# Kernel optimization log

Hardware: AMD Instinct MI355X
Metric: run time of the kernel (lower is better)

## Reference

```python
import jax, jax.numpy as jnp
import numpy as np

B, T, EMB, H1, H2, NL, LMAX, VOCAB = 32, 20, 32, 64, 128, 4, 1024, 85
EPS = 1e-5

def _lengths():
    # ragged per-structure atom counts, max = 1024 (fixes pad length), sum = 24832
    return 1024 - np.arange(B) * 16

def _lstm(x, Wih0, Whh0, b0, WihS, WhhS, bS):
    """NL-layer batch-first LSTM, torch gate order (i,f,g,o), initial h/c = ones
    (matching the torch code's ones init states). Returns stacked final
    (h, c) per layer, each (NL, batch, hidden)."""
    n = x.shape[0]
    hidden = Whh0.shape[1]
    h_fin, c_fin = [], []
    inp = x
    for l in range(NL):
        Wih = Wih0 if l == 0 else WihS[l - 1]
        Whh = Whh0 if l == 0 else WhhS[l - 1]
        bb = b0 if l == 0 else bS[l - 1]
        xg = jnp.einsum('bti,gi->btg', inp, Wih) + bb  # (n, t, 4*hidden)
        init = (jnp.ones((n, hidden), x.dtype), jnp.ones((n, hidden), x.dtype))
        def step(carry, xt, Whh=Whh):
            h, c = carry
            g = xt + h @ Whh.T
            i, f, gg, o = jnp.split(g, 4, axis=-1)
            c = jax.nn.sigmoid(f) * c + jax.nn.sigmoid(i) * jnp.tanh(gg)
            h = jax.nn.sigmoid(o) * jnp.tanh(c)
            return (h, c), h
        (hT, cT), hs = jax.lax.scan(step, init, jnp.swapaxes(xg, 0, 1))
        inp = jnp.swapaxes(hs, 0, 1)
        h_fin.append(hT)
        c_fin.append(cT)
    return jnp.stack(h_fin), jnp.stack(c_fin)

def _bn_rows(x, g, b):
    # BatchNorm1d(batch_size) applied to x.T in torch: per-row (per-structure)
    # normalization over the feature axis, training-mode (biased var).
    m = x.mean(1, keepdims=True)
    v = x.var(1, keepdims=True)
    return (x - m) * jax.lax.rsqrt(v + EPS) * g[:, None] + b[:, None]

def setup_inputs():
    lengths = _lengths()
    N = int(lengths.sum())
    ks = jax.random.split(jax.random.key(0), 32)
    ki = iter(range(32))
    def nrm(shape, s):
        return s * jax.random.normal(ks[next(ki)], shape, jnp.float32)
    return {
        'neighbor_atom_batch': jax.random.randint(ks[next(ki)], (N * T,), 0, VOCAB, dtype=jnp.int32),
        'neighbors_distan_batch': jax.random.normal(ks[next(ki)], (N * T,), jnp.float32),
        'structure_num_bacth': jnp.asarray(lengths, jnp.int32),
        'batch_idx': jnp.asarray(np.repeat(np.arange(B), lengths), jnp.int32),
        'pos_idx': jnp.asarray(np.concatenate([np.arange(l) for l in lengths]), jnp.int32),
        'embed_w': nrm((VOCAB, EMB), 0.02),
        'l1_Wih0': nrm((4 * H1, EMB), 0.05), 'l1_Whh0': nrm((4 * H1, H1), 0.05), 'l1_b0': nrm((4 * H1,), 0.02),
        'l1_Wih': nrm((NL - 1, 4 * H1, H1), 0.05), 'l1_Whh': nrm((NL - 1, 4 * H1, H1), 0.05), 'l1_b': nrm((NL - 1, 4 * H1), 0.02),
        'l2_Wih0': nrm((4 * H2, H1), 0.05), 'l2_Whh0': nrm((4 * H2, H2), 0.05), 'l2_b0': nrm((4 * H2,), 0.02),
        'l2_Wih': nrm((NL - 1, 4 * H2, H2), 0.05), 'l2_Whh': nrm((NL - 1, 4 * H2, H2), 0.05), 'l2_b': nrm((NL - 1, 4 * H2), 0.02),
        'bn2_g': jnp.ones((B,), jnp.float32), 'bn2_b': jnp.zeros((B,), jnp.float32),
        'bn3_g': jnp.ones((B,), jnp.float32), 'bn3_b': jnp.zeros((B,), jnp.float32),
        'w1': nrm((128, 128), 0.1), 'b1': 0.1 * jnp.ones((128,), jnp.float32),
        'w2': nrm((64, 128), 0.1), 'b2': 0.1 * jnp.ones((64,), jnp.float32),
        'w22': nrm((64, 64), 0.1), 'b22': 0.1 * jnp.ones((64,), jnp.float32),
        'w3': nrm((32, 64), 0.1), 'b3': 0.1 * jnp.ones((32,), jnp.float32),
        'w4': nrm((32, 32), 0.1), 'b4': 0.1 * jnp.ones((32,), jnp.float32),
        'w5': nrm((16, 32), 0.1), 'b5': 0.1 * jnp.ones((16,), jnp.float32),
    }

def reference(neighbor_atom_batch, neighbors_distan_batch, structure_num_bacth,
              batch_idx, pos_idx, embed_w,
              l1_Wih0, l1_Whh0, l1_b0, l1_Wih, l1_Whh, l1_b,
              l2_Wih0, l2_Whh0, l2_b0, l2_Wih, l2_Whh, l2_b,
              bn2_g, bn2_b, bn3_g, bn3_b,
              w1, b1, w2, b2, w22, b22, w3, b3, w4, b4, w5, b5):
    # NOTE: neighbors_distan_batch is an argument of the torch forward but is
    # never used by its body; we keep it for signature fidelity.
    # embed, then scale each embedding row by its own integer atom id (as torch does)
    x = embed_w[neighbor_atom_batch] * neighbor_atom_batch.astype(jnp.float32)[:, None]
    x = x.reshape(-1, T, EMB)                       # (N, 20, 32)
    hT, cT = _lstm(x, l1_Wih0, l1_Whh0, l1_b0, l1_Wih, l1_Whh, l1_b)
    d = hT.mean(0) + cT.mean(0)                     # (N, 64)
    # ragged split by structure_num_bacth + pad_sequence -> (B, LMAX, 64), zero padded
    padded = jnp.zeros((B, LMAX, H1), d.dtype).at[batch_idx, pos_idx].set(d)
    # BatchNorm1d(batch_size): channel dim is the structure index -> stats over (len, feat)
    m = padded.mean((1, 2), keepdims=True)
    v = padded.var((1, 2), keepdims=True)
    padded = (padded - m) * jax.lax.rsqrt(v + EPS) * bn2_g[:, None, None] + bn2_b[:, None, None]
    _, cT2 = _lstm(padded, l2_Wih0, l2_Whh0, l2_b0, l2_Wih, l2_Whh, l2_b)
    d = cT2.mean(0)                                 # (B, 128) mean of final cell states
    d = _bn_rows(d, bn3_g, bn3_b)
    d = jax.nn.relu(d @ w1.T + b1)
    d = jax.nn.relu(d @ w2.T + b2)
    d = _bn_rows(d, bn3_g, bn3_b)                   # same BN layer reused, as in torch
    d = jax.nn.relu(d @ w22.T + b22)
    d = jax.nn.relu(d @ w3.T + b3)
    d = jax.nn.relu(d @ w4.T + b4)
    d = d @ w5.T + b5                               # (B, 16)
    return jax.nn.relu(d.sum(1))                    # (B,)
```

## Files before the change

### kernel.cpp

```cpp
#include <hip/hip_runtime.h>


typedef _Float16 f16x8  __attribute__((ext_vector_type(8)));
typedef float    f32x4  __attribute__((ext_vector_type(4)));

#define DEVI static __device__ __forceinline__

constexpr int   T1c   = 20;
constexpr int   EMBc  = 32;
constexpr int   H1c   = 64;
constexpr int   LMAXc = 1024;
constexpr int   VOCABc= 85;
constexpr int   Ntot  = 24832;
constexpr int   NTc   = Ntot * T1c;
constexpr int   R2c   = 32 * LMAXc;
constexpr float EPSc  = 1e-5f;

DEVI float sigm(float x)   { return 1.f / (1.f + __expf(-x)); }
DEVI float tanhf_(float x) { return 1.f - 2.f / (1.f + __expf(2.f * x)); }

DEVI void barrier_lds() {
    asm volatile("s_waitcnt lgkmcnt(0)\n\ts_barrier" ::: "memory");
}
DEVI void drain_vmem() {
    asm volatile("s_waitcnt vmcnt(0)" ::: "memory");
}

__global__ void __launch_bounds__(256)
k_prepw1(const float* __restrict__ Wih0, const float* __restrict__ Whh0,
         const float* __restrict__ WihS, const float* __restrict__ WhhS,
         _Float16* __restrict__ out)
{
    int i = blockIdx.x * 256 + threadIdx.x;
    if (i >= 4 * 256 * 128) return;
    int l = i >> 15, rem = i & 32767, r = rem >> 7, k = rem & 127;
    float v;
    if (l == 0) {
        if (k < 32)      v = Wih0[r * 32 + k];
        else if (k < 64) v = 0.f;
        else             v = Whh0[r * 64 + (k - 64)];
    } else {
        if (k < 64)      v = WihS[((l - 1) * 256 + r) * 64 + k];
        else             v = WhhS[((l - 1) * 256 + r) * 64 + (k - 64)];
    }
    out[i] = (_Float16)v;
}

__global__ void __launch_bounds__(256)
k_prepw2(const float* __restrict__ Wih0, const float* __restrict__ WihS,
         const float* __restrict__ Whh0, const float* __restrict__ WhhS,
         _Float16* __restrict__ wih, _Float16* __restrict__ whh,
         int* __restrict__ flags)
{
    int i = blockIdx.x * 256 + threadIdx.x;
    if (i < 512) flags[i] = (i < 256) ? 0 : 0x7fffffff;
    if (i >= 2 * 4 * 512 * 128) return;
    int half = i >> 18, rem = i & 262143;
    int l = rem >> 16, r = (rem >> 7) & 511, k = rem & 127;
    if (half == 0) {
        float v = (l == 0) ? ((k < 64) ? Wih0[r * 64 + k] : 0.f)
                           : WihS[((l - 1) * 512 + r) * 128 + k];
        wih[rem] = (_Float16)v;
    } else {
        float v = (l == 0) ? Whh0[r * 128 + k]
                           : WhhS[((l - 1) * 512 + r) * 128 + k];
        whh[rem] = (_Float16)v;
    }
}

__global__ void __launch_bounds__(256)
k_scan1all(const int* __restrict__ atoms, const float* __restrict__ ew,
           const _Float16* __restrict__ W16all,
           const float* __restrict__ b0, const float* __restrict__ bS,
           _Float16* __restrict__ seq, float* __restrict__ dacc)
{
    constexpr int SX = 136;
    __shared__ alignas(16) _Float16 xh[32 * SX];
    __shared__ float ewl[VOCABc * EMBc];
    __shared__ int   aidl[32 * T1c];

    const int tid  = threadIdx.x;
    const int lane = tid & 63;
    const int wv   = tid >> 6;
    const int l16  = lane & 15;
    const int quad = lane >> 4;
    const int n0   = blockIdx.x * 32;
    const int d    = wv * 16 + l16;

    for (int i = tid; i < VOCABc * EMBc; i += 256) ewl[i] = ew[i];
    for (int i = tid; i < 32 * T1c; i += 256) aidl[i] = atoms[n0 * T1c + i];

    float daccv[2][4];
#pragma unroll
    for (int mt = 0; mt < 2; ++mt)
#pragma unroll
        for (int r = 0; r < 4; ++r) daccv[mt][r] = 0.f;

    __syncthreads();

#pragma unroll 1
    for (int l = 0; l < 4; ++l) {
        const _Float16* W16  = W16all + (size_t)l * 256 * 128;
        const float*    bptr = (l == 0) ? b0 : bS + (l - 1) * 256;

        float bias[4];
#pragma unroll
        for (int g = 0; g < 4; ++g) bias[g] = bptr[g * 64 + d];

        f16x8 wF[4][4];
#pragma unroll
        for (int kc = 0; kc < 4; ++kc) {
            const int kb = kc * 32 + quad * 8;
#pragma unroll
            for (int g = 0; g < 4; ++g)
                wF[kc][g] = *(const f16x8*)&W16[(size_t)(g * 64 + d) * 128 + kb];
        }

        f32x4 c[2];
        c[0] = {1.f, 1.f, 1.f, 1.f};
        c[1] = {1.f, 1.f, 1.f, 1.f};

        drain_vmem();
        __syncthreads();

#pragma unroll
        for (int mt = 0; mt < 2; ++mt)
#pragma unroll
            for (int r = 0; r < 4; ++r)
                xh[(mt * 16 + quad * 4 + r) * SX + 64 + d] = (_Float16)1.0f;
        if (l == 0)
            for (int idx = tid; idx < 32 * 32; idx += 256) {
                int s = idx >> 5, e = idx & 31;
                xh[s * SX + 32 + e] = (_Float16)0.f;
            }

#pragma unroll 1
        for (int t = 0; t < T1c; ++t) {
            if (l == 0) {
                for (int idx = tid; idx < 32 * 32; idx += 256) {
                    int s = idx >> 5, e = idx & 31;
                    int id = aidl[s * T1c + t];
                    xh[s * SX + e] = (_Float16)(ewl[id * EMBc + e] * (float)id);
                }
            } else {
                for (int idx = tid; idx < 32 * 8; idx += 256) {
                    int s = idx >> 3, k8 = idx & 7;
                    *(f16x8*)&xh[s * SX + k8 * 8] =
                        *(const f16x8*)&seq[((size_t)(n0 + s) * T1c + t) * H1c + k8 * 8];
                }
            }
            __syncthreads();

            f32x4 acc[2][4];
#pragma unroll
            for (int mt = 0; mt < 2; ++mt)
#pragma unroll
                for (int g = 0; g < 4; ++g)
                    acc[mt][g] = {bias[g], bias[g], bias[g], bias[g]};

#pragma unroll
            for (int kc = 0; kc < 4; ++kc) {
                const int kb = kc * 32 + quad * 8;
                f16x8 ah[2];
#pragma unroll
                for (int mt = 0; mt < 2; ++mt)
                    ah[mt] = *(const f16x8*)&xh[(mt * 16 + l16) * SX + kb];
#pragma unroll
                for (int g = 0; g < 4; ++g)
#pragma unroll
                    for (int mt = 0; mt < 2; ++mt)
                        acc[mt][g] = __builtin_amdgcn_mfma_f32_16x16x32_f16(ah[mt], wF[kc][g], acc[mt][g], 0, 0, 0);
            }
            __syncthreads();

#pragma unroll
            for (int mt = 0; mt < 2; ++mt)
#pragma unroll
                for (int r = 0; r < 4; ++r) {
                    float iv = sigm(acc[mt][0][r]);
                    float fv = sigm(acc[mt][1][r]);
                    float gv = tanhf_(acc[mt][2][r]);
                    float ov = sigm(acc[mt][3][r]);
                    float cv = fv * c[mt][r] + iv * gv;
                    c[mt][r] = cv;
                    float hv = ov * tanhf_(cv);
                    _Float16 hf = (_Float16)hv;
                    int s = mt * 16 + quad * 4 + r;
                    xh[s * SX + 64 + d] = hf;
                    if (l < 3)
                        seq[((size_t)(n0 + s) * T1c + t) * H1c + d] = hf;
                    if (t == T1c - 1)
                        daccv[mt][r] += 0.25f * (hv + cv);
                }
        }
    }
#pragma unroll
    for (int mt = 0; mt < 2; ++mt)
#pragma unroll
        for (int r = 0; r < 4; ++r) {
            int s = mt * 16 + quad * 4 + r;
            dacc[(size_t)(n0 + s) * H1c + d] = daccv[mt][r];
        }
}

__global__ void __launch_bounds__(256)
k_bn2_stats(const int* __restrict__ lens, const float* __restrict__ dacc,
            float* __restrict__ stats)
{
    int b = blockIdx.x;
    int off = 0;
    for (int i = 0; i < b; ++i) off += lens[i];
    int len = lens[b];
    const float* base = dacc + (long)off * H1c;
    float s = 0.f, ss = 0.f;
    int total = len * H1c;
    for (int i = threadIdx.x; i < total; i += 256) { float v = base[i]; s += v; ss += v * v; }
    __shared__ float rs[256], rss[256];
    rs[threadIdx.x] = s; rss[threadIdx.x] = ss;
    __syncthreads();
    for (int st = 128; st > 0; st >>= 1) {
        if (threadIdx.x < st) { rs[threadIdx.x] += rs[threadIdx.x + st]; rss[threadIdx.x] += rss[threadIdx.x + st]; }
        __syncthreads();
    }
    if (threadIdx.x == 0) {
        float m = rs[0] / (float)(LMAXc * H1c);
        float v = rss[0] / (float)(LMAXc * H1c) - m * m;
        stats[b]      = m;
        stats[32 + b] = rsqrtf(fmaxf(v, 0.f) + EPSc);
        stats[64 + b] = (float)off;
    }
}

__global__ void __launch_bounds__(256)
k_bn2_apply(const float* __restrict__ dacc, const float* __restrict__ stats,
            const int* __restrict__ lens, const float* __restrict__ g,
            const float* __restrict__ bb, _Float16* __restrict__ outA)
{
    int i = blockIdx.x * 256 + threadIdx.x;
    if (i >= R2c * 128) return;
    int rr = i >> 7, k = i & 127;
    int b = rr >> 10, p = rr & 1023;
    float y = 0.f;
    if (k < H1c) {
        int off = (int)stats[64 + b];
        float x = (p < lens[b]) ? dacc[(off + p) * H1c + k] : 0.f;
        y = (x - stats[b]) * stats[32 + b] * g[b] + bb[b];
    }
    outA[(size_t)(p * 32 + b) * 128 + k] = (_Float16)y;
}

DEVI float qsel(f32x4 a, int quad) {
    float t01 = (quad & 1) ? a[1] : a[0];
    float t23 = (quad & 1) ? a[3] : a[2];
    return (quad & 2) ? t23 : t01;
}

DEVI void spin_ge(const int* fl, int lane, int need)
{
    for (;;) {
        int f = 0x7fffffff;
        if (lane < 8)
            asm volatile("global_load_dword %0, %1, off sc0 sc1\n\ts_waitcnt vmcnt(0)"
                         : "+v"(f) : "v"(fl) : "memory");
        if (__all(f >= need)) break;
    }
}

#define STEP(T, PAR, R, F)                                                          \
  {                                                                                 \
    f32x4 acc[4];                                                                   \
    _Pragma("unroll") for (int g4 = 0; g4 < 4; ++g4)                                \
        acc[g4] = {bia[g4], bia[g4], bia[g4], bia[g4]};                             \
    _Pragma("unroll") for (int kc = 0; kc < 4; ++kc) {                              \
        f16x8 ax = *(const f16x8*)&xp[PAR][(l16 & 3) * SH + kc * 32 + quad * 8];    \
        _Pragma("unroll") for (int g4 = 0; g4 < 4; ++g4)                            \
            acc[g4] = __builtin_amdgcn_mfma_f32_16x16x32_f16(ax, wI[g4][kc], acc[g4], 0, 0, 0); \
    }                                                                               \
    _Pragma("unroll") for (int kc = 0; kc < 4; ++kc) {                              \
        f16x8 ah = *(const f16x8*)&av[PAR][(l16 & 3) * SH + kc * 32 + quad * 8];    \
        _Pragma("unroll") for (int g4 = 0; g4 < 4; ++g4)                            \
            acc[g4] = __builtin_amdgcn_mfma_f32_16x16x32_f16(ah, wH[g4][kc], acc[g4], 0, 0, 0); \
    }                                                                               \
    asm volatile("s_waitcnt vmcnt(4)" ::: "memory");                                \
    __builtin_amdgcn_sched_barrier(0);                                              \
    if (lane == 0) {                                                                \
        int fv = (T) - 1;                                                           \
        asm volatile("global_store_dword %0, %1, off sc0 sc1"                       \
                     :: "v"(myflag), "v"(fv) : "memory");                           \
    }                                                                               \
    *(unsigned*)&xp[PAR ^ 1][csam * SH + 2 * coff] = R;                             \
    float gi = qsel(acc[0], quad);                                                  \
    float gf = qsel(acc[1], quad);                                                  \
    float gg = qsel(acc[2], quad);                                                  \
    float go = qsel(acc[3], quad);                                                  \
    float cv = sigm(gf) * cst + sigm(gi) * tanhf_(gg);                              \
    cst = cv;                                                                       \
    float hv = sigm(go) * tanhf_(cv);                                               \
    _Float16 hf = (_Float16)hv;                                                     \
    av[PAR ^ 1][quad * SH + cell] = hf;                                             \
    {                                                                               \
        int need = ((T) <= LMAXc - 4) ? (T) + 4 : 0;                                \
        if (!__all(lane >= 8 || F >= need)) spin_ge(sflag, lane, need);             \
    }                                                                               \
    if (l == 0)                                                                     \
        asm volatile("global_load_dword %0, %1, off" : "=v"(R) : "v"(xq) : "memory"); \
    else                                                                            \
        asm volatile("global_load_dword %0, %1, off sc0 sc1" : "=v"(R) : "v"(xq) : "memory"); \
    if ((T) < LMAXc - 4) xq += xstep;                                               \
    {   unsigned hb = (unsigned)__builtin_bit_cast(unsigned short, hf);             \
        asm volatile("global_store_short %0, %1, off sc0 sc1"                       \
                     :: "v"(hp), "v"(hb) : "memory"); }                             \
    hp += 512;                                                                      \
    if (lane < 8)                                                                   \
        asm volatile("global_load_dword %0, %1, off sc0 sc1"                        \
                     : "+v"(F) : "v"(sflag) : "memory");                            \
    barrier_lds();                                                                  \
  }

__global__ void
__attribute__((amdgpu_flat_work_group_size(512, 512), amdgpu_waves_per_eu(2, 2)))
k_scan2p(const _Float16* __restrict__ seqA,
         const _Float16* __restrict__ wihAll,
         const _Float16* __restrict__ whhAll,
         const float* __restrict__ b0,
         const float* __restrict__ bS,
         _Float16* __restrict__ hbuf,
         int* __restrict__ flags,
         float* __restrict__ c2)
{
    constexpr int SH = 144;
    __shared__ alignas(16) _Float16 av[2][4 * SH];
    __shared__ alignas(16) _Float16 xp[2][4 * SH];

    const int bx   = blockIdx.x;
    const int l    = bx & 3;
    const int g    = bx >> 2;
    const int tid  = threadIdx.x;
    const int lane = tid & 63;
    const int w    = tid >> 6;
    const int l16  = lane & 15;
    const int quad = lane >> 4;
    const int cell = w * 16 + l16;

    const _Float16* Wih = wihAll + (size_t)l * 512 * 128;
    const _Float16* Whh = whhAll + (size_t)l * 512 * 128;
    const float*   bptr = (l == 0) ? b0 : bS + (l - 1) * 512;

    f16x8 wI[4][4], wH[4][4];
    float bia[4];
#pragma unroll
    for (int g4 = 0; g4 < 4; ++g4) {
#pragma unroll
        for (int kc = 0; kc < 4; ++kc) {
            wI[g4][kc] = *(const f16x8*)&Wih[(size_t)(g4 * 128 + cell) * 128 + kc * 32 + quad * 8];
            wH[g4][kc] = *(const f16x8*)&Whh[(size_t)(g4 * 128 + cell) * 128 + kc * 32 + quad * 8];
        }
        bia[g4] = bptr[g4 * 128 + cell];
    }
#pragma unroll
    for (int g4 = 0; g4 < 4; ++g4) {
#pragma unroll
        for (int kc = 0; kc < 4; ++kc) {
            asm volatile("" : "+a"(wI[g4][kc]));
            asm volatile("" : "+a"(wH[g4][kc]));
        }
        asm volatile("" : "+v"(bia[g4]));
    }
    drain_vmem();
    __builtin_amdgcn_sched_barrier(0);

    const int ci   = tid & 255;
    const int csam = ci >> 6;
    const int coff = ci & 63;

    const unsigned* xq;
    int xstep;
    if (l == 0) {
        xq    = (const unsigned*)seqA + ((size_t)(g * 4 + csam)) * 64 + coff;
        xstep = 32 * 64;
    } else {
        xq    = (const unsigned*)(hbuf + ((size_t)((l - 1) * 8 + g)) * (LMAXc * 512)) + ci;
        xstep = 256;
    }

    _Float16*  hp     = hbuf + ((size_t)(l * 8 + g)) * (LMAXc * 512) + quad * 128 + cell;
    int*       myflag = flags + (l * 8 + g) * 8 + w;
    const int* sflag  = (l == 0) ? (flags + 256 + (lane & 7))
                                 : (flags + ((l - 1) * 8 + g) * 8 + (lane & 7));

    { int s = tid >> 7, e = tid & 127; av[0][s * SH + e] = (_Float16)1.0f; }
    float cst = 1.f;

    unsigned rA, rB;
    int fpreA = 0, fpreB = 0;

    spin_ge(sflag, lane, 1);
    if (l == 0) asm volatile("global_load_dword %0, %1, off" : "=v"(rA) : "v"(xq) : "memory");
    else        asm volatile("global_load_dword %0, %1, off sc0 sc1" : "=v"(rA) : "v"(xq) : "memory");
    drain_vmem();
    __builtin_amdgcn_sched_barrier(0);
    *(unsigned*)&xp[0][csam * SH + 2 * coff] = rA;

    spin_ge(sflag, lane, 2);
    {
        const unsigned* p1 = xq + xstep;
        if (l == 0) asm volatile("global_load_dword %0, %1, off" : "=v"(rA) : "v"(p1) : "memory");
        else        asm volatile("global_load_dword %0, %1, off sc0 sc1" : "=v"(rA) : "v"(p1) : "memory");
    }
    drain_vmem();
    __builtin_amdgcn_sched_barrier(0);

    spin_ge(sflag, lane, 3);
    {
        const unsigned* p2 = xq + 2 * xstep;
        if (l == 0) asm volatile("global_load_dword %0, %1, off" : "=v"(rB) : "v"(p2) : "memory");
        else        asm volatile("global_load_dword %0, %1, off sc0 sc1" : "=v"(rB) : "v"(p2) : "memory");
    }
    if (lane < 8) {
        asm volatile("global_load_dword %0, %1, off sc0 sc1" : "+v"(fpreA) : "v"(sflag) : "memory");
        asm volatile("global_load_dword %0, %1, off sc0 sc1" : "+v"(fpreB) : "v"(sflag) : "memory");
    }
    xq += 3 * (size_t)xstep;
    __syncthreads();

#pragma unroll 1
    for (int t = 0; t < LMAXc; t += 2) {
        STEP(t,     0, rA, fpreA)
        STEP(t + 1, 1, rB, fpreB)
    }

    drain_vmem();
    if (lane == 0) {
        int fin = LMAXc;
        asm volatile("global_store_dword %0, %1, off sc0 sc1"
                     :: "v"(myflag), "v"(fin) : "memory");
    }
    c2[(size_t)l * 4096 + (g * 4 + quad) * 128 + cell] = 0.25f * cst;
}

DEVI void bn_rows_dev(float* X, int K, const float* g, const float* bb,
                      float* mv, int tid)
{
    __syncthreads();
    if (tid < 32) {
        float s = 0.f, ss = 0.f;
        const float* r = X + tid * K;
        for (int k = 0; k < K; ++k) { float v = r[k]; s += v; ss += v * v; }
        float m = s / (float)K;
        float vv = ss / (float)K - m * m;
        mv[tid]      = m;
        mv[32 + tid] = rsqrtf(fmaxf(vv, 0.f) + EPSc);
    }
    __syncthreads();
    for (int i = tid; i < 32 * K; i += 256) {
        int b = i / K;
        X[i] = (X[i] - mv[b]) * mv[32 + b] * g[b] + bb[b];
    }
    __syncthreads();
}

DEVI void lin_dev(const float* X, int K, const float* W, const float* bias,
                  int NO, float* Y, int relu, int tid)
{
    __syncthreads();
    for (int i = tid; i < 32 * NO; i += 256) {
        int b = i / NO, j = i - b * NO;
        float a = bias[j];
        const float* xr = X + b * K;
        const float* wr = W + j * K;
        for (int k = 0; k < K; ++k) a += xr[k] * wr[k];
        Y[i] = relu ? fmaxf(a, 0.f) : a;
    }
    __syncthreads();
}

__global__ void __launch_bounds__(256)
k_head(const float* __restrict__ c2, const float* __restrict__ g3, const float* __restrict__ bb3,
       const float* w1, const float* b1, const float* w2, const float* b2,
       const float* w22, const float* b22, const float* w3, const float* b3,
       const float* w4, const float* b4, const float* w5, const float* b5,
       float* __restrict__ out)
{
    __shared__ float A[32 * 128];
    __shared__ float Bf[32 * 128];
    __shared__ float mv[64];
    const int tid = threadIdx.x;

    for (int i = tid; i < 32 * 128; i += 256)
        A[i] = c2[i] + c2[4096 + i] + c2[8192 + i] + c2[12288 + i];
    bn_rows_dev(A, 128, g3, bb3, mv, tid);
    lin_dev(A, 128, w1, b1, 128, Bf, 1, tid);
    lin_dev(Bf, 128, w2, b2, 64, A, 1, tid);
    bn_rows_dev(A, 64, g3, bb3, mv, tid);
    lin_dev(A, 64, w22, b22, 64, Bf, 1, tid);
    lin_dev(Bf, 64, w3, b3, 32, A, 1, tid);
    lin_dev(A, 32, w4, b4, 32, Bf, 1, tid);
    lin_dev(Bf, 32, w5, b5, 16, A, 0, tid);
    if (tid < 32) {
        float s = 0.f;
        for (int j = 0; j < 16; ++j) s += A[tid * 16 + j];
        out[tid] = fmaxf(s, 0.f);
    }
}

extern "C" void kernel_launch(void* const* d_in, const int* in_sizes, int n_in,
                              void* d_out, int out_size, void* d_ws, size_t ws_size,
                              hipStream_t stream)
{
    const int*   atoms  = (const int*)d_in[0];
    const int*   lens   = (const int*)d_in[2];
    const float* embw   = (const float*)d_in[5];
    const float* l1Wih0 = (const float*)d_in[6];
    const float* l1Whh0 = (const float*)d_in[7];
    const float* l1b0   = (const float*)d_in[8];
    const float* l1Wih  = (const float*)d_in[9];
    const float* l1Whh  = (const float*)d_in[10];
    const float* l1b    = (const float*)d_in[11];
    const float* l2Wih0 = (const float*)d_in[12];
    const float* l2Whh0 = (const float*)d_in[13];
    const float* l2b0   = (const float*)d_in[14];
    const float* l2Wih  = (const float*)d_in[15];
    const float* l2Whh  = (const float*)d_in[16];
    const float* l2b    = (const float*)d_in[17];
    const float* bn2g   = (const float*)d_in[18];
    const float* bn2b   = (const float*)d_in[19];
    const float* bn3g   = (const float*)d_in[20];
    const float* bn3b   = (const float*)d_in[21];
    const float* w1  = (const float*)d_in[22]; const float* b1  = (const float*)d_in[23];
    const float* w2  = (const float*)d_in[24]; const float* b2  = (const float*)d_in[25];
    const float* w22 = (const float*)d_in[26]; const float* b22 = (const float*)d_in[27];
    const float* w3  = (const float*)d_in[28]; const float* b3  = (const float*)d_in[29];
    const float* w4  = (const float*)d_in[30]; const float* b4  = (const float*)d_in[31];
    const float* w5  = (const float*)d_in[32]; const float* b5  = (const float*)d_in[33];
    float* out = (float*)d_out;

    char* base = (char*)d_ws;
    size_t off = 0;
    auto take = [&](size_t bytes) -> char* {
        char* p = base + off;
        off = (off + bytes + 255) & ~(size_t)255;
        return p;
    };
    _Float16* seq1f  = (_Float16*)take((size_t)NTc * H1c * 2);
    float*    dacc   = (float*)take((size_t)Ntot * H1c * 4);
    _Float16* wcomb1 = (_Float16*)take((size_t)4 * 256 * 128 * 2);
    _Float16* wih16  = (_Float16*)take((size_t)4 * 512 * 128 * 2);
    _Float16* whh16  = (_Float16*)take((size_t)4 * 512 * 128 * 2);
    _Float16* seqA   = (_Float16*)take((size_t)R2c * 128 * 2);
    _Float16* hbuf   = (_Float16*)take((size_t)4 * 8 * LMAXc * 512 * 2);
    int*      flags  = (int*)take(512 * sizeof(int));
    float*    stats  = (float*)take(1024);
    float*    c2     = (float*)take((size_t)4 * 32 * 128 * 4);

    k_prepw1<<<(4 * 256 * 128 + 255) / 256, 256, 0, stream>>>(l1Wih0, l1Whh0, l1Wih, l1Whh, wcomb1);
    k_prepw2<<<(2 * 4 * 512 * 128 + 255) / 256, 256, 0, stream>>>(l2Wih0, l2Wih, l2Whh0, l2Whh, wih16, whh16, flags);

    k_scan1all<<<Ntot / 32, 256, 0, stream>>>(atoms, embw, wcomb1, l1b0, l1b, seq1f, dacc);

    k_bn2_stats<<<32, 256, 0, stream>>>(lens, dacc, stats);
    k_bn2_apply<<<(R2c * 128 + 255) / 256, 256, 0, stream>>>(dacc, stats, lens, bn2g, bn2b, seqA);

    k_scan2p<<<32, 512, 0, stream>>>(seqA, wih16, whh16, l2b0, l2b, hbuf, flags, c2);

    k_head<<<1, 256, 0, stream>>>(c2, bn3g, bn3b, w1, b1, w2, b2, w22, b22,
                                  w3, b3, w4, b4, w5, b5, out);

    (void)in_sizes; (void)n_in; (void)out_size; (void)ws_size;
}
```

Baseline: 1.795 ms.

## Split LSTM2 recurrent gate matmul across 16 waves with LDS gate exchange

Doubles the k_scan2p workgroup from 8 to 16 waves, so each wave computes two 16-column gate tiles instead of four per step. Each wave holds half as many weight registers. Gate pre-activations are written to a shared LDS array and regathered per cell, and the bias is added from LDS. The flags are resized to 16 per group so the cross-layer pipeline still works. This shortens the MFMA chain per step on the serial recurrence, at the cost of an extra barrier and LDS round-trip every timestep and more waves polling flags.

```diff
diff --git a/kernel.cpp b/kernel.cpp
--- a/kernel.cpp
+++ b/kernel.cpp
@@ -53,7 +53,7 @@
          int* __restrict__ flags)
 {
     int i = blockIdx.x * 256 + threadIdx.x;
-    if (i < 512) flags[i] = (i < 256) ? 0 : 0x7fffffff;
+    if (i < 1024) flags[i] = (i < 512) ? 0 : 0x7fffffff;
     if (i >= 2 * 4 * 512 * 128) return;
     int half = i >> 18, rem = i & 262143;
     int l = rem >> 16, r = (rem >> 7) & 511, k = rem & 127;
@@ -259,7 +259,7 @@
 {
     for (;;) {
         int f = 0x7fffffff;
-        if (lane < 8)
+        if (lane < 16)
             asm volatile("global_load_dword %0, %1, off sc0 sc1\n\ts_waitcnt vmcnt(0)"
                          : "+v"(f) : "v"(fl) : "memory");
         if (__all(f >= need)) break;
@@ -268,19 +268,19 @@
 
 #define STEP(T, PAR, R, F)                                                          \
   {                                                                                 \
-    f32x4 acc[4];                                                                   \
-    _Pragma("unroll") for (int g4 = 0; g4 < 4; ++g4)                                \
-        acc[g4] = {bia[g4], bia[g4], bia[g4], bia[g4]};                             \
+    f32x4 acc0 = {0.f, 0.f, 0.f, 0.f}, acc1 = {0.f, 0.f, 0.f, 0.f};                 \
     _Pragma("unroll") for (int kc = 0; kc < 4; ++kc) {                              \
         f16x8 ax = *(const f16x8*)&xp[PAR][(l16 & 3) * SH + kc * 32 + quad * 8];    \
-        _Pragma("unroll") for (int g4 = 0; g4 < 4; ++g4)                            \
-            acc[g4] = __builtin_amdgcn_mfma_f32_16x16x32_f16(ax, wI[g4][kc], acc[g4], 0, 0, 0); \
+        acc0 = __builtin_amdgcn_mfma_f32_16x16x32_f16(ax, wB[0][kc], acc0, 0, 0, 0);\
+        acc1 = __builtin_amdgcn_mfma_f32_16x16x32_f16(ax, wB[1][kc], acc1, 0, 0, 0);\
     }                                                                               \
     _Pragma("unroll") for (int kc = 0; kc < 4; ++kc) {                              \
         f16x8 ah = *(const f16x8*)&av[PAR][(l16 & 3) * SH + kc * 32 + quad * 8];    \
-        _Pragma("unroll") for (int g4 = 0; g4 < 4; ++g4)                            \
-            acc[g4] = __builtin_amdgcn_mfma_f32_16x16x32_f16(ah, wH[g4][kc], acc[g4], 0, 0, 0); \
+        acc0 = __builtin_amdgcn_mfma_f32_16x16x32_f16(ah, wB[0][4 + kc], acc0, 0, 0, 0);\
+        acc1 = __builtin_amdgcn_mfma_f32_16x16x32_f16(ah, wB[1][4 + kc], acc1, 0, 0, 0);\
     }                                                                               \
+    pre[quad * 520 + wn0 + l16]      = qsel(acc0, quad);                            \
+    pre[quad * 520 + wn0 + 16 + l16] = qsel(acc1, quad);                            \
     asm volatile("s_waitcnt vmcnt(4)" ::: "memory");                                \
     __builtin_amdgcn_sched_barrier(0);                                              \
     if (lane == 0) {                                                                \
@@ -289,18 +289,19 @@
                      :: "v"(myflag), "v"(fv) : "memory");                           \
     }                                                                               \
     *(unsigned*)&xp[PAR ^ 1][csam * SH + 2 * coff] = R;                             \
-    float gi = qsel(acc[0], quad);                                                  \
-    float gf = qsel(acc[1], quad);                                                  \
-    float gg = qsel(acc[2], quad);                                                  \
-    float go = qsel(acc[3], quad);                                                  \
+    barrier_lds();                                                                  \
+    float gi = pre[gs * 520 + gc]       + bL[gc];                                   \
+    float gf = pre[gs * 520 + 128 + gc] + bL[128 + gc];                             \
+    float gg = pre[gs * 520 + 256 + gc] + bL[256 + gc];                             \
+    float go = pre[gs * 520 + 384 + gc] + bL[384 + gc];                             \
     float cv = sigm(gf) * cst + sigm(gi) * tanhf_(gg);                              \
     cst = cv;                                                                       \
     float hv = sigm(go) * tanhf_(cv);                                               \
     _Float16 hf = (_Float16)hv;                                                     \
-    av[PAR ^ 1][quad * SH + cell] = hf;                                             \
+    av[PAR ^ 1][gs * SH + gc] = hf;                                                 \
     {                                                                               \
         int need = ((T) <= LMAXc - 4) ? (T) + 4 : 0;                                \
-        if (!__all(lane >= 8 || F >= need)) spin_ge(sflag, lane, need);             \
+        if (!__all(lane >= 16 || F >= need)) spin_ge(sflag, lane, need);            \
     }                                                                               \
     if (l == 0)                                                                     \
         asm volatile("global_load_dword %0, %1, off" : "=v"(R) : "v"(xq) : "memory"); \
@@ -311,14 +312,14 @@
         asm volatile("global_store_short %0, %1, off sc0 sc1"                       \
                      :: "v"(hp), "v"(hb) : "memory"); }                             \
     hp += 512;                                                                      \
-    if (lane < 8)                                                                   \
+    if (lane < 16)                                                                  \
         asm volatile("global_load_dword %0, %1, off sc0 sc1"                        \
                      : "+v"(F) : "v"(sflag) : "memory");                            \
     barrier_lds();                                                                  \
   }
 
 __global__ void
-__attribute__((amdgpu_flat_work_group_size(512, 512), amdgpu_waves_per_eu(2, 2)))
+__attribute__((amdgpu_flat_work_group_size(1024, 1024), amdgpu_waves_per_eu(4, 4)))
 k_scan2p(const _Float16* __restrict__ seqA,
          const _Float16* __restrict__ wihAll,
          const _Float16* __restrict__ whhAll,
@@ -331,6 +332,8 @@
     constexpr int SH = 144;
     __shared__ alignas(16) _Float16 av[2][4 * SH];
     __shared__ alignas(16) _Float16 xp[2][4 * SH];
+    __shared__ float pre[4 * 520];
+    __shared__ float bL[512];
 
     const int bx   = blockIdx.x;
     const int l    = bx & 3;
@@ -340,32 +343,32 @@
     const int w    = tid >> 6;
     const int l16  = lane & 15;
     const int quad = lane >> 4;
-    const int cell = w * 16 + l16;
+    const int wn0  = w * 32;
+    const int gp   = tid & 511;
+    const int gs   = gp >> 7;
+    const int gc   = gp & 127;
 
     const _Float16* Wih = wihAll + (size_t)l * 512 * 128;
     const _Float16* Whh = whhAll + (size_t)l * 512 * 128;
     const float*   bptr = (l == 0) ? b0 : bS + (l - 1) * 512;
 
-    f16x8 wI[4][4], wH[4][4];
-    float bia[4];
-#pragma unroll
-    for (int g4 = 0; g4 < 4; ++g4) {
+    if (tid < 512) bL[tid] = bptr[tid];
+
+    f16x8 wB[2][8];
+#pragma unroll
+    for (int nt = 0; nt < 2; ++nt) {
+        const int n = wn0 + nt * 16 + l16;
 #pragma unroll
         for (int kc = 0; kc < 4; ++kc) {
-            wI[g4][kc] = *(const f16x8*)&Wih[(size_t)(g4 * 128 + cell) * 128 + kc * 32 + quad * 8];
-            wH[g4][kc] = *(const f16x8*)&Whh[(size_t)(g4 * 128 + cell) * 128 + kc * 32 + quad * 8];
+            wB[nt][kc]     = *(const f16x8*)&Wih[(size_t)n * 128 + kc * 32 + quad * 8];
+            wB[nt][4 + kc] = *(const f16x8*)&Whh[(size_t)n * 128 + kc * 32 + quad * 8];
         }
-        bia[g4] = bptr[g4 * 128 + cell];
-    }
-#pragma unroll
-    for (int g4 = 0; g4 < 4; ++g4) {
-#pragma unroll
-        for (int kc = 0; kc < 4; ++kc) {
-            asm volatile("" : "+a"(wI[g4][kc]));
-            asm volatile("" : "+a"(wH[g4][kc]));
-        }
-        asm volatile("" : "+v"(bia[g4]));
-    }
+    }
+#pragma unroll
+    for (int nt = 0; nt < 2; ++nt)
+#pragma unroll
+        for (int k = 0; k < 8; ++k)
+            asm volatile("" : "+a"(wB[nt][k]));
     drain_vmem();
     __builtin_amdgcn_sched_barrier(0);
 
@@ -383,12 +386,12 @@
         xstep = 256;
     }
 
-    _Float16*  hp     = hbuf + ((size_t)(l * 8 + g)) * (LMAXc * 512) + quad * 128 + cell;
-    int*       myflag = flags + (l * 8 + g) * 8 + w;
-    const int* sflag  = (l == 0) ? (flags + 256 + (lane & 7))
-                                 : (flags + ((l - 1) * 8 + g) * 8 + (lane & 7));
-
-    { int s = tid >> 7, e = tid & 127; av[0][s * SH + e] = (_Float16)1.0f; }
+    _Float16*  hp     = hbuf + ((size_t)(l * 8 + g)) * (LMAXc * 512) + gp;
+    int*       myflag = flags + (l * 8 + g) * 16 + w;
+    const int* sflag  = (l == 0) ? (flags + 512 + (lane & 15))
+                                 : (flags + ((l - 1) * 8 + g) * 16 + (lane & 15));
+
+    if (tid < 512) av[0][gs * SH + gc] = (_Float16)1.0f;
     float cst = 1.f;
 
     unsigned rA, rB;
@@ -416,7 +419,7 @@
         if (l == 0) asm volatile("global_load_dword %0, %1, off" : "=v"(rB) : "v"(p2) : "memory");
         else        asm volatile("global_load_dword %0, %1, off sc0 sc1" : "=v"(rB) : "v"(p2) : "memory");
     }
-    if (lane < 8) {
+    if (lane < 16) {
         asm volatile("global_load_dword %0, %1, off sc0 sc1" : "+v"(fpreA) : "v"(sflag) : "memory");
         asm volatile("global_load_dword %0, %1, off sc0 sc1" : "+v"(fpreB) : "v"(sflag) : "memory");
     }
@@ -435,7 +438,8 @@
         asm volatile("global_store_dword %0, %1, off sc0 sc1"
                      :: "v"(myflag), "v"(fin) : "memory");
     }
-    c2[(size_t)l * 4096 + (g * 4 + quad) * 128 + cell] = 0.25f * cst;
+    if (tid < 512)
+        c2[(size_t)l * 4096 + (g * 4 + gs) * 128 + gc] = 0.25f * cst;
 }
 
 DEVI void bn_rows_dev(float* X, int K, const float* g, const float* bb,
@@ -548,7 +552,7 @@
     _Float16* whh16  = (_Float16*)take((size_t)4 * 512 * 128 * 2);
     _Float16* seqA   = (_Float16*)take((size_t)R2c * 128 * 2);
     _Float16* hbuf   = (_Float16*)take((size_t)4 * 8 * LMAXc * 512 * 2);
-    int*      flags  = (int*)take(512 * sizeof(int));
+    int*      flags  = (int*)take(1024 * sizeof(int));
     float*    stats  = (float*)take(1024);
     float*    c2     = (float*)take((size_t)4 * 32 * 128 * 4);
 
@@ -560,7 +564,7 @@
     k_bn2_stats<<<32, 256, 0, stream>>>(lens, dacc, stats);
     k_bn2_apply<<<(R2c * 128 + 255) / 256, 256, 0, stream>>>(dacc, stats, lens, bn2g, bn2b, seqA);
 
-    k_scan2p<<<32, 512, 0, stream>>>(seqA, wih16, whh16, l2b0, l2b, hbuf, flags, c2);
+    k_scan2p<<<32, 1024, 0, stream>>>(seqA, wih16, whh16, l2b0, l2b, hbuf, flags, c2);
 
     k_head<<<1, 256, 0, stream>>>(c2, bn3g, bn3b, w1, b1, w2, b2, w22, b22,
                                   w3, b3, w4, b4, w5, b5, out);
```

Result: slower. 2.313 ms (+28.9%).
